# Optimization experiments

Measured on AMD Instinct MI355X. Metric: run time of the kernel, lower is better.

## Reference

```python
import jax, jax.numpy as jnp
import numpy as np

NUM_LEAVES = 256
EPS = 1e-6
SHARPNESS = 1.0   # init_sharpness, non-trainable buffer
BIAS_SHIFT = -2.0


def _generalized_gcd(w1, w2, lambd):
    # lambd: per-node bias -> andness via sigmoid; broadcast over batch
    lam = jax.nn.sigmoid(lambd)
    a = jnp.abs(w1) + EPS
    b = jnp.abs(w2) + EPS
    return lam * jnp.minimum(a, b) + (1.0 - lam) * jnp.maximum(a, b)


def setup_inputs() -> dict:
    key = jax.random.key(0)
    ks = jax.random.split(key, 6)
    B, L = 65536, NUM_LEAVES
    x = jax.random.normal(ks[0], (B, L), jnp.float32)
    # xavier-like scale for the leaf projection
    W_leaf = jax.random.normal(ks[1], (L, L), jnp.float32) * (1.0 / np.sqrt(L))
    weights = jax.random.uniform(ks[2], (L - 1, 2), jnp.float32, 0.5, 1.5)
    biases = jax.random.uniform(ks[3], (L - 1,), jnp.float32) * 0.1
    w_out = jax.random.normal(ks[4], (1, 1), jnp.float32)
    b_out = jnp.full((1,), 0.5, jnp.float32)
    return {"x": x, "W_leaf": W_leaf, "weights": weights,
            "biases": biases, "w_out": w_out, "b_out": b_out}


def reference(x, W_leaf, weights, biases, w_out, b_out):
    # InputToLeafFC: sigmoid(sharpness * (x @ W^T + bias_shift))
    leaf = jax.nn.sigmoid(SHARPNESS * (x @ W_leaf.T + BIAS_SHIFT))  # (B, L)

    # The original pops two nodes from the front of the queue and appends the
    # result; for a power-of-two leaf count this is exactly a level-by-level
    # pairwise tree reduction, with node weights consumed in order.
    cur = leaf
    off = 0
    n = cur.shape[1]
    while n > 1:  # log2(L) levels, each fully vectorized over (batch, pairs)
        m = n // 2
        w = weights[off:off + m]   # (m, 2)
        b = biases[off:off + m]    # (m,)
        left = cur[:, 0::2] * w[:, 0]
        right = cur[:, 1::2] * w[:, 1]
        cur = _generalized_gcd(left, right, b)  # (B, m)
        off += m
        n = m
    # fc_out: Linear(1,1) then sigmoid -> (B, 1)
    return jax.nn.sigmoid(cur * w_out[0, 0] + b_out[0])
```

## Files before the change

kernel.cpp:

```cpp
#include <hip/hip_runtime.h>
#include <stdint.h>


#define EPS 1e-6f
#define LOG2E 1.44269504088896340736f

typedef __attribute__((ext_vector_type(8))) short short8;
typedef __attribute__((ext_vector_type(4))) short short4_t;
typedef __attribute__((ext_vector_type(4))) float float4_t;

__device__ __forceinline__ float fast_sigmoid(float z) {
    float e = __builtin_amdgcn_exp2f(-z * LOG2E);
    return __builtin_amdgcn_rcpf(1.0f + e);
}

__device__ __forceinline__ short f2bf(float f) {
    uint32_t u = __builtin_bit_cast(uint32_t, f);
    u += 0x7FFFu + ((u >> 16) & 1u);
    return (short)(u >> 16);
}

__device__ __forceinline__ short8 pack8(float4 a, float4 b) {
    short8 s;
    s[0] = f2bf(a.x); s[1] = f2bf(a.y); s[2] = f2bf(a.z); s[3] = f2bf(a.w);
    s[4] = f2bf(b.x); s[5] = f2bf(b.y); s[6] = f2bf(b.z); s[7] = f2bf(b.w);
    return s;
}

__device__ __forceinline__ float ggcd(float l, float r, float lam) {
    float a = fabsf(l) + EPS;
    float b = fabsf(r) + EPS;
    float mn = fminf(a, b);
    float mx = fmaxf(a, b);
    return fmaf(lam, mn - mx, mx);
}

__device__ __forceinline__ void stage_tile(const float* __restrict__ Wl,
                                           short* dst, int kt, int tid) {
    const int m  = tid & 15;
    const int g  = (tid >> 4) & 3;
    const int jb = tid >> 4;
    const int cpos2h = (m + 4 * g) & 15;
    const int cpos = cpos2h >> 1;
    const int h    = cpos2h & 1;
    #pragma unroll
    for (int i = 0; i < 8; ++i) {
        int j   = i * 32 + jb;
        int col = kt * 64 + ((cpos ^ (j & 7)) << 3) + h * 4;
        int src = ((j & 15) << 4) | (j >> 4);
        float4 w4 = *(const float4*)&Wl[src * 256 + col];
        short4_t s4;
        s4.x = f2bf(w4.x); s4.y = f2bf(w4.y); s4.z = f2bf(w4.z); s4.w = f2bf(w4.w);
        *(short4_t*)((char*)dst + j * 128 + cpos2h * 8) = s4;
    }
}

__device__ __forceinline__ void tree_reduce(float4_t acc[16], int c0,
                                            const float4* pv, float res[4]) {
    #pragma unroll
    for (int t = 0; t < 16; ++t) {
        #pragma unroll
        for (int r = 0; r < 4; ++r) acc[t][r] = fast_sigmoid(acc[t][r] - 2.0f);
    }
    #pragma unroll
    for (int tp = 0; tp < 8; ++tp) {
        float4 p = pv[c0 * 8 + tp];
        #pragma unroll
        for (int r = 0; r < 4; ++r)
            acc[tp][r] = ggcd(acc[2*tp][r] * p.x, acc[2*tp+1][r] * p.y, p.z);
    }
    #pragma unroll
    for (int tp = 0; tp < 4; ++tp) {
        float4 p = pv[128 + c0 * 4 + tp];
        #pragma unroll
        for (int r = 0; r < 4; ++r)
            acc[tp][r] = ggcd(acc[2*tp][r] * p.x, acc[2*tp+1][r] * p.y, p.z);
    }
    #pragma unroll
    for (int tp = 0; tp < 2; ++tp) {
        float4 p = pv[192 + c0 * 2 + tp];
        #pragma unroll
        for (int r = 0; r < 4; ++r)
            acc[tp][r] = ggcd(acc[2*tp][r] * p.x, acc[2*tp+1][r] * p.y, p.z);
    }
    {
        float4 p = pv[224 + c0];
        #pragma unroll
        for (int r = 0; r < 4; ++r)
            res[r] = ggcd(acc[0][r] * p.x, acc[1][r] * p.y, p.z);
    }
}

__global__ __launch_bounds__(512, 4)
void btln_main(const float* __restrict__ x, const float* __restrict__ Wl,
               const float* __restrict__ wts, const float* __restrict__ bia,
               const float* __restrict__ wout, const float* __restrict__ bout,
               float* __restrict__ out) {
    __shared__ short Wt[2][16384];
    __shared__ float4 pv[256];

    const int tid  = threadIdx.x;
    const int lane = tid & 63;
    const int wv   = tid >> 6;
    const int c0   = lane & 15;
    const int q    = lane >> 4;

    if (tid < 255) {
        pv[tid] = make_float4(wts[2 * tid], wts[2 * tid + 1],
                              fast_sigmoid(bia[tid]), 0.f);
    } else if (tid == 255) {
        pv[255] = make_float4(0.f, 0.f, 0.f, 0.f);
    }

    stage_tile(Wl, Wt[0], 0, tid);

    const int rowbase = blockIdx.x * 128 + wv * 16;
    const float* xr = x + (size_t)(rowbase + c0) * 256;

    float4 r0 = *(const float4*)(xr + q * 8);
    float4 r1 = *(const float4*)(xr + q * 8 + 4);
    float4 r2 = *(const float4*)(xr + 32 + q * 8);
    float4 r3 = *(const float4*)(xr + 32 + q * 8 + 4);
    short8 afc0 = pack8(r0, r1);
    short8 afc1 = pack8(r2, r3);

    float4_t acc[16];
    #pragma unroll
    for (int t = 0; t < 16; ++t) acc[t] = (float4_t){0.f, 0.f, 0.f, 0.f};

    __syncthreads();

    const int vx = c0 & 7;

#define KSTEP(kt, LAST)                                                       \
    {                                                                         \
        const short* cur = Wt[(kt) & 1];                                      \
        float4 n0, n1, n2, n3;                                                \
        if (!(LAST)) {                          \
            const float* xn = xr + ((kt) + 1) * 64;                           \
            n0 = *(const float4*)(xn + q * 8);                                \
            n1 = *(const float4*)(xn + q * 8 + 4);                            \
            n2 = *(const float4*)(xn + 32 + q * 8);                           \
            n3 = *(const float4*)(xn + 32 + q * 8 + 4);                       \
        }                                                                     \
        _Pragma("unroll")                                                     \
        for (int t = 0; t < 16; ++t) {                                        \
            const short* base = &cur[(t * 16 + c0) * 64];                     \
            short8 bf0 = *(const short8*)&base[(q ^ vx) * 8];                 \
            short8 bf1 = *(const short8*)&base[((q + 4) ^ vx) * 8];           \
            acc[t] = __builtin_amdgcn_mfma_f32_16x16x32_bf16(                 \
                afc0, bf0, acc[t], 0, 0, 0);                                  \
            acc[t] = __builtin_amdgcn_mfma_f32_16x16x32_bf16(                 \
                afc1, bf1, acc[t], 0, 0, 0);                                  \
        }                                                                     \
        __builtin_amdgcn_sched_barrier(0);        \
        if (!(LAST)) {                                                        \
            stage_tile(Wl, Wt[((kt) + 1) & 1], (kt) + 1, tid);                \
            afc0 = pack8(n0, n1);                                             \
            afc1 = pack8(n2, n3);                                             \
            __syncthreads();                         \
        }                                                                     \
    }

    KSTEP(0, 0)
    KSTEP(1, 0)
    KSTEP(2, 0)
    KSTEP(3, 1)
#undef KSTEP

    float res[4];
    tree_reduce(acc, c0, pv, res);

    const int offs[4] = {240, 248, 252, 254};
    #pragma unroll
    for (int k = 0; k < 4; ++k) {
        float4 p = pv[offs[k] + (c0 >> (k + 1))];
        bool isLeft = ((c0 >> k) & 1) == 0;
        #pragma unroll
        for (int r = 0; r < 4; ++r) {
            float other = __shfl_xor(res[r], 1 << k, 64);
            float lf = isLeft ? res[r] : other;
            float rt = isLeft ? other  : res[r];
            res[r] = ggcd(lf * p.x, rt * p.y, p.z);
        }
    }

    if (c0 == 0) {
        const float wo = wout[0];
        const float bo = bout[0];
        #pragma unroll
        for (int r = 0; r < 4; ++r)
            out[rowbase + q * 4 + r] = fast_sigmoid(fmaf(res[r], wo, bo));
    }
}

extern "C" void kernel_launch(void* const* d_in, const int* in_sizes, int n_in,
                              void* d_out, int out_size, void* d_ws, size_t ws_size,
                              hipStream_t stream) {
    const float* x   = (const float*)d_in[0];
    const float* Wl  = (const float*)d_in[1];
    const float* wts = (const float*)d_in[2];
    const float* bia = (const float*)d_in[3];
    const float* wo  = (const float*)d_in[4];
    const float* bo  = (const float*)d_in[5];
    float* out = (float*)d_out;

    const int rows = out_size;
    dim3 grid(rows / 128), block(512);
    btln_main<<<grid, block, 0, stream>>>(x, Wl, wts, bia, wo, bo, out);
}
```

Baseline: 121.1 us.

## Split W tile staging into two halves interleaved with MFMA loop

The W staging is reorganised so each thread loads 8 consecutive floats per row and writes 16-byte bf16 chunks, replacing the eight float4/short4 stores per tile. The next tile's global loads are issued in two halves, before and between the two halves of the MFMA loop, and the LDS writes are deferred. This is meant to hide global-load latency for the weight tile behind matrix work instead of stalling after the full MFMA loop. It raises register pressure from holding prefetched float4s and relies on sched_barrier to keep the ordering.

```diff
diff --git a/kernel.cpp b/kernel.cpp
--- a/kernel.cpp
+++ b/kernel.cpp
@@ -33,26 +33,6 @@
     float mn = fminf(a, b);
     float mx = fmaxf(a, b);
     return fmaf(lam, mn - mx, mx);
-}
-
-__device__ __forceinline__ void stage_tile(const float* __restrict__ Wl,
-                                           short* dst, int kt, int tid) {
-    const int m  = tid & 15;
-    const int g  = (tid >> 4) & 3;
-    const int jb = tid >> 4;
-    const int cpos2h = (m + 4 * g) & 15;
-    const int cpos = cpos2h >> 1;
-    const int h    = cpos2h & 1;
-    #pragma unroll
-    for (int i = 0; i < 8; ++i) {
-        int j   = i * 32 + jb;
-        int col = kt * 64 + ((cpos ^ (j & 7)) << 3) + h * 4;
-        int src = ((j & 15) << 4) | (j >> 4);
-        float4 w4 = *(const float4*)&Wl[src * 256 + col];
-        short4_t s4;
-        s4.x = f2bf(w4.x); s4.y = f2bf(w4.y); s4.z = f2bf(w4.z); s4.w = f2bf(w4.w);
-        *(short4_t*)((char*)dst + j * 128 + cpos2h * 8) = s4;
-    }
 }
 
 __device__ __forceinline__ void tree_reduce(float4_t acc[16], int c0,
@@ -105,6 +85,16 @@
     const int c0   = lane & 15;
     const int q    = lane >> 4;
 
+    const int scpos = tid & 7;
+    const int sjj   = tid >> 3;
+    const int scol  = (scpos ^ (sjj & 7)) << 3;
+    const int j0 = sjj,       j1 = 64 + sjj,  j2 = 128 + sjj, j3 = 192 + sjj;
+    const int ssrc0 = ((j0 & 15) << 4) | (j0 >> 4);
+    const int ssrc1 = ((j1 & 15) << 4) | (j1 >> 4);
+    const int ssrc2 = ((j2 & 15) << 4) | (j2 >> 4);
+    const int ssrc3 = ((j3 & 15) << 4) | (j3 >> 4);
+    const int wslot = sjj * 128 + scpos * 16;
+
     if (tid < 255) {
         pv[tid] = make_float4(wts[2 * tid], wts[2 * tid + 1],
                               fast_sigmoid(bia[tid]), 0.f);
@@ -112,7 +102,22 @@
         pv[255] = make_float4(0.f, 0.f, 0.f, 0.f);
     }
 
-    stage_tile(Wl, Wt[0], 0, tid);
+    {
+        const float* wsrc = Wl + scol;
+        char* wb = (char*)&Wt[0][0] + wslot;
+        float4 a0 = *(const float4*)(wsrc + ssrc0 * 256);
+        float4 b0 = *(const float4*)(wsrc + ssrc0 * 256 + 4);
+        float4 a1 = *(const float4*)(wsrc + ssrc1 * 256);
+        float4 b1 = *(const float4*)(wsrc + ssrc1 * 256 + 4);
+        float4 a2 = *(const float4*)(wsrc + ssrc2 * 256);
+        float4 b2 = *(const float4*)(wsrc + ssrc2 * 256 + 4);
+        float4 a3 = *(const float4*)(wsrc + ssrc3 * 256);
+        float4 b3 = *(const float4*)(wsrc + ssrc3 * 256 + 4);
+        *(short8*)(wb)         = pack8(a0, b0);
+        *(short8*)(wb + 8192)  = pack8(a1, b1);
+        *(short8*)(wb + 16384) = pack8(a2, b2);
+        *(short8*)(wb + 24576) = pack8(a3, b3);
+    }
 
     const int rowbase = blockIdx.x * 128 + wv * 16;
     const float* xr = x + (size_t)(rowbase + c0) * 256;
@@ -132,33 +137,57 @@
 
     const int vx = c0 & 7;
 
+#define MFMA_T(t)                                                             \
+    {                                                                         \
+        const short* base = &cur[((t) * 16 + c0) * 64];                       \
+        short8 bf0 = *(const short8*)&base[(q ^ vx) * 8];                     \
+        short8 bf1 = *(const short8*)&base[((q + 4) ^ vx) * 8];               \
+        acc[t] = __builtin_amdgcn_mfma_f32_16x16x32_bf16(                     \
+            afc0, bf0, acc[t], 0, 0, 0);                                      \
+        acc[t] = __builtin_amdgcn_mfma_f32_16x16x32_bf16(                     \
+            afc1, bf1, acc[t], 0, 0, 0);                                      \
+    }
+
 #define KSTEP(kt, LAST)                                                       \
     {                                                                         \
         const short* cur = Wt[(kt) & 1];                                      \
-        float4 n0, n1, n2, n3;                                                \
-        if (!(LAST)) {                          \
-            const float* xn = xr + ((kt) + 1) * 64;                           \
+        char* wbn = (char*)&Wt[((kt) + 1) & 1][0] + wslot;                    \
+        const float* wsrc = Wl + ((kt) + 1) * 64 + scol;                      \
+        float4 s0, s1, s2, s3, n0, n1, n2, n3;                                \
+        if (!(LAST)) {                         \
+            s0 = *(const float4*)(wsrc + ssrc0 * 256);                        \
+            s1 = *(const float4*)(wsrc + ssrc0 * 256 + 4);                    \
+            s2 = *(const float4*)(wsrc + ssrc1 * 256);                        \
+            s3 = *(const float4*)(wsrc + ssrc1 * 256 + 4);                    \
+            const float* xn = xr + ((kt) + 1) * 64;         \
             n0 = *(const float4*)(xn + q * 8);                                \
             n1 = *(const float4*)(xn + q * 8 + 4);                            \
             n2 = *(const float4*)(xn + 32 + q * 8);                           \
             n3 = *(const float4*)(xn + 32 + q * 8 + 4);                       \
+            __builtin_amdgcn_sched_barrier(0);                                \
         }                                                                     \
         _Pragma("unroll")                                                     \
-        for (int t = 0; t < 16; ++t) {                                        \
-            const short* base = &cur[(t * 16 + c0) * 64];                     \
-            short8 bf0 = *(const short8*)&base[(q ^ vx) * 8];                 \
-            short8 bf1 = *(const short8*)&base[((q + 4) ^ vx) * 8];           \
-            acc[t] = __builtin_amdgcn_mfma_f32_16x16x32_bf16(                 \
-                afc0, bf0, acc[t], 0, 0, 0);                                  \
-            acc[t] = __builtin_amdgcn_mfma_f32_16x16x32_bf16(                 \
-                afc1, bf1, acc[t], 0, 0, 0);                                  \
+        for (int t = 0; t < 8; ++t) MFMA_T(t)                                 \
+        __builtin_amdgcn_sched_barrier(0);                                    \
+        float4 u0, u1, u2, u3;                                                \
+        if (!(LAST)) {                         \
+            *(short8*)(wbn)        = pack8(s0, s1);                           \
+            *(short8*)(wbn + 8192) = pack8(s2, s3);                           \
+            u0 = *(const float4*)(wsrc + ssrc2 * 256);                        \
+            u1 = *(const float4*)(wsrc + ssrc2 * 256 + 4);                    \
+            u2 = *(const float4*)(wsrc + ssrc3 * 256);                        \
+            u3 = *(const float4*)(wsrc + ssrc3 * 256 + 4);                    \
+            __builtin_amdgcn_sched_barrier(0);                                \
         }                                                                     \
-        __builtin_amdgcn_sched_barrier(0);        \
-        if (!(LAST)) {                                                        \
-            stage_tile(Wl, Wt[((kt) + 1) & 1], (kt) + 1, tid);                \
+        _Pragma("unroll")                                                     \
+        for (int t = 8; t < 16; ++t) MFMA_T(t)                                \
+        __builtin_amdgcn_sched_barrier(0);                                    \
+        if (!(LAST)) {                              \
+            *(short8*)(wbn + 16384) = pack8(u0, u1);                          \
+            *(short8*)(wbn + 24576) = pack8(u2, u3);                          \
             afc0 = pack8(n0, n1);                                             \
             afc1 = pack8(n2, n3);                                             \
-            __syncthreads();                         \
+            __syncthreads();                  \
         }                                                                     \
     }
 
@@ -167,6 +196,7 @@
     KSTEP(2, 0)
     KSTEP(3, 1)
 #undef KSTEP
+#undef MFMA_T
 
     float res[4];
     tree_reduce(acc, c0, pv, res);
```

New measurement: 116.3 us. 3.9% less time.

## Stage full bf16 W_leaf in LDS upfront with 1024-thread blocks, drop per-step syncs

Applied to the files above, without the earlier changes.

Each block now converts and stages the whole 256x256 W_leaf into LDS (128KB) once at the start, instead of double-buffering 64-column tiles per k-step. This removes the per-k-step stage and __syncthreads barriers. Blocks double to 1024 threads covering 256 rows, so half as many blocks each redo the W conversion. The cost is much larger LDS per block, which limits occupancy to about one block per CU, and a larger upfront staging phase that no longer overlaps with MFMA work.

```diff
diff --git a/kernel.cpp b/kernel.cpp
--- a/kernel.cpp
+++ b/kernel.cpp
@@ -35,26 +35,6 @@
     return fmaf(lam, mn - mx, mx);
 }
 
-__device__ __forceinline__ void stage_tile(const float* __restrict__ Wl,
-                                           short* dst, int kt, int tid) {
-    const int m  = tid & 15;
-    const int g  = (tid >> 4) & 3;
-    const int jb = tid >> 4;
-    const int cpos2h = (m + 4 * g) & 15;
-    const int cpos = cpos2h >> 1;
-    const int h    = cpos2h & 1;
-    #pragma unroll
-    for (int i = 0; i < 8; ++i) {
-        int j   = i * 32 + jb;
-        int col = kt * 64 + ((cpos ^ (j & 7)) << 3) + h * 4;
-        int src = ((j & 15) << 4) | (j >> 4);
-        float4 w4 = *(const float4*)&Wl[src * 256 + col];
-        short4_t s4;
-        s4.x = f2bf(w4.x); s4.y = f2bf(w4.y); s4.z = f2bf(w4.z); s4.w = f2bf(w4.w);
-        *(short4_t*)((char*)dst + j * 128 + cpos2h * 8) = s4;
-    }
-}
-
 __device__ __forceinline__ void tree_reduce(float4_t acc[16], int c0,
                                             const float4* pv, float res[4]) {
     #pragma unroll
@@ -91,12 +71,12 @@
     }
 }
 
-__global__ __launch_bounds__(512, 4)
+__global__ __launch_bounds__(1024, 4)
 void btln_main(const float* __restrict__ x, const float* __restrict__ Wl,
                const float* __restrict__ wts, const float* __restrict__ bia,
                const float* __restrict__ wout, const float* __restrict__ bout,
                float* __restrict__ out) {
-    __shared__ short Wt[2][16384];
+    __shared__ short Wt[4][16384];
     __shared__ float4 pv[256];
 
     const int tid  = threadIdx.x;
@@ -112,9 +92,30 @@
         pv[255] = make_float4(0.f, 0.f, 0.f, 0.f);
     }
 
-    stage_tile(Wl, Wt[0], 0, tid);
-
-    const int rowbase = blockIdx.x * 128 + wv * 16;
+    {
+        const int scpos = tid & 7;
+        const int sj    = (tid >> 3) & 63;
+        const int half  = tid >> 9;
+        const int jA    = sj + 128 * half;
+        const int jB    = jA + 64;
+        const int colx  = (scpos ^ (sj & 7)) << 3;
+        const int srcA  = ((jA & 15) << 4) | (jA >> 4);
+        const int srcB  = ((jB & 15) << 4) | (jB >> 4);
+        #pragma unroll
+        for (int kt = 0; kt < 4; ++kt) {
+            const float* pA = Wl + srcA * 256 + kt * 64 + colx;
+            const float* pB = Wl + srcB * 256 + kt * 64 + colx;
+            float4 a0 = *(const float4*)(pA);
+            float4 a1 = *(const float4*)(pA + 4);
+            float4 b0 = *(const float4*)(pB);
+            float4 b1 = *(const float4*)(pB + 4);
+            char* base = (char*)&Wt[kt][0] + scpos * 16;
+            *(short8*)(base + jA * 128) = pack8(a0, a1);
+            *(short8*)(base + jB * 128) = pack8(b0, b1);
+        }
+    }
+
+    const int rowbase = blockIdx.x * 256 + wv * 16;
     const float* xr = x + (size_t)(rowbase + c0) * 256;
 
     float4 r0 = *(const float4*)(xr + q * 8);
@@ -132,9 +133,20 @@
 
     const int vx = c0 & 7;
 
+#define MFMA_T(t)                                                             \
+    {                                                                         \
+        const short* base = &cur[((t) * 16 + c0) * 64];                       \
+        short8 bf0 = *(const short8*)&base[(q ^ vx) * 8];                     \
+        short8 bf1 = *(const short8*)&base[((q + 4) ^ vx) * 8];               \
+        acc[t] = __builtin_amdgcn_mfma_f32_16x16x32_bf16(                     \
+            afc0, bf0, acc[t], 0, 0, 0);                                      \
+        acc[t] = __builtin_amdgcn_mfma_f32_16x16x32_bf16(                     \
+            afc1, bf1, acc[t], 0, 0, 0);                                      \
+    }
+
 #define KSTEP(kt, LAST)                                                       \
     {                                                                         \
-        const short* cur = Wt[(kt) & 1];                                      \
+        const short* cur = &Wt[kt][0];                                        \
         float4 n0, n1, n2, n3;                                                \
         if (!(LAST)) {                          \
             const float* xn = xr + ((kt) + 1) * 64;                           \
@@ -144,22 +156,12 @@
             n3 = *(const float4*)(xn + 32 + q * 8 + 4);                       \
         }                                                                     \
         _Pragma("unroll")                                                     \
-        for (int t = 0; t < 16; ++t) {                                        \
-            const short* base = &cur[(t * 16 + c0) * 64];                     \
-            short8 bf0 = *(const short8*)&base[(q ^ vx) * 8];                 \
-            short8 bf1 = *(const short8*)&base[((q + 4) ^ vx) * 8];           \
-            acc[t] = __builtin_amdgcn_mfma_f32_16x16x32_bf16(                 \
-                afc0, bf0, acc[t], 0, 0, 0);                                  \
-            acc[t] = __builtin_amdgcn_mfma_f32_16x16x32_bf16(                 \
-                afc1, bf1, acc[t], 0, 0, 0);                                  \
-        }                                                                     \
-        __builtin_amdgcn_sched_barrier(0);        \
+        for (int t = 0; t < 16; ++t) MFMA_T(t)                                \
         if (!(LAST)) {                                                        \
-            stage_tile(Wl, Wt[((kt) + 1) & 1], (kt) + 1, tid);                \
             afc0 = pack8(n0, n1);                                             \
             afc1 = pack8(n2, n3);                                             \
-            __syncthreads();                         \
         }                                                                     \
+        __builtin_amdgcn_sched_barrier(0);       \
     }
 
     KSTEP(0, 0)
@@ -167,6 +169,7 @@
     KSTEP(2, 0)
     KSTEP(3, 1)
 #undef KSTEP
+#undef MFMA_T
 
     float res[4];
     tree_reduce(acc, c0, pv, res);
@@ -206,6 +209,6 @@
     float* out = (float*)d_out;
 
     const int rows = out_size;
-    dim3 grid(rows / 128), block(512);
+    dim3 grid(rows / 256), block(1024);
     btln_main<<<grid, block, 0, stream>>>(x, Wl, wts, bia, wo, bo, out);
 }
```

After: 114.6 us. 1.06x faster.
